# Optimization experiments

Measured on AMD Instinct MI355X. Metric: run time of the kernel, lower is better.

The kernel has to match this reference:

```python
import jax, jax.numpy as jnp
import numpy as np

NUM_HEADS = 8
HEAD_DIM = 64
SCALE = HEAD_DIM ** -0.5
EPS = 1e-5
STRIDE = (2, 2)


def _layernorm(x, g, b):
    mu = x.mean(-1, keepdims=True)
    var = x.var(-1, keepdims=True)
    return (x - mu) * jax.lax.rsqrt(var + EPS) * g + b


def _pool(t, convw, ln_g, ln_b, H):
    # t: (B, T, nh, 1 + H*H, d); depthwise-conv pool of spatial tokens, cls kept as-is,
    # LayerNorm over per-head channel dim applied after re-attaching cls (matches torch).
    B, T, nh, N, d = t.shape
    t = t.reshape(B * T, nh, N, d)
    cls_tok, body = t[:, :, :1], t[:, :, 1:]
    xs = body.reshape(B * T * nh, H, H, d)
    xs = jax.lax.conv_general_dilated(
        xs, convw, window_strides=STRIDE, padding=((1, 1), (1, 1)),
        dimension_numbers=('NHWC', 'HWIO', 'NHWC'), feature_group_count=d)
    Ho, Wo = xs.shape[1], xs.shape[2]
    xs = xs.reshape(B * T, nh, Ho * Wo, d)
    xs = jnp.concatenate([cls_tok, xs], axis=2)
    xs = _layernorm(xs, ln_g, ln_b)
    return xs.reshape(B, T, nh, Ho * Wo + 1, d), (Ho, Wo)


def _lin(t, w, b):
    # (B, T, nh, n, d) -> fold heads -> Linear(nh*d -> nh*d) -> unfold heads
    B, T, nh, n, d = t.shape
    y = t.transpose(0, 1, 3, 2, 4).reshape(B * T, n, nh * d)
    y = y @ w.T + b
    return y.reshape(B, T, n, nh, d).transpose(0, 1, 3, 2, 4)


def reference(x, x_ref, w_q, b_q, w_k, b_k, w_v, b_v, w_proj, b_proj,
              convw_q, convw_k, convw_v, ln_g_q, ln_b_q, ln_g_k, ln_b_k,
              ln_g_v, ln_b_v, rel_pos_h, rel_pos_w, hw_shape):
    B, T1, N, C = x.shape
    T2 = x_ref.shape[1]
    nh, d = NUM_HEADS, C // NUM_HEADS
    H = int(hw_shape)
    # pool_first: split heads before pooling;  q from x, k = v from x_ref
    q = x.reshape(B, T1, N, nh, d).transpose(0, 1, 3, 2, 4)
    kv = x_ref.reshape(B, T2, N, nh, d).transpose(0, 1, 3, 2, 4)
    q, q_shape = _pool(q, convw_q, ln_g_q, ln_b_q, H)
    k, k_shape = _pool(kv, convw_k, ln_g_k, ln_b_k, H)
    v, _ = _pool(kv, convw_v, ln_g_v, ln_b_v, H)
    q = _lin(q, w_q, b_q)
    k = _lin(k, w_k, b_k)
    v = _lin(v, w_v, b_v)
    # b t nh n d -> b nh (t n) d
    q = q.transpose(0, 2, 1, 3, 4).reshape(B, nh, -1, d)
    k = k.transpose(0, 2, 1, 3, 4).reshape(B, nh, -1, d)
    v = v.transpose(0, 2, 1, 3, 4).reshape(B, nh, -1, d)
    attn = jnp.einsum('bhqd,bhkd->bhqk', q * SCALE, k)
    # inline spatial relative position bias (uses UNSCALED q, as in torch source)
    qh, qw = q_shape
    kh, kw = k_shape
    dh = (np.arange(qh)[:, None] * max(kh / qh, 1.0)
          - np.arange(kh)[None, :] * max(qh / kh, 1.0)
          + (kh - 1) * max(qh / kh, 1.0)).astype(np.int32)
    dw = (np.arange(qw)[:, None] * max(kw / qw, 1.0)
          - np.arange(kw)[None, :] * max(qw / kw, 1.0)
          + (kw - 1) * max(qw / kw, 1.0)).astype(np.int32)
    Rh = rel_pos_h[dh]  # (qh, kh, d)
    Rw = rel_pos_w[dw]  # (qw, kw, d)
    r_q = q[:, :, 1:].reshape(B, nh, qh, qw, d)
    rel_h = jnp.einsum('byhwc,hkc->byhwk', r_q, Rh)
    rel_w = jnp.einsum('byhwc,wkc->byhwk', r_q, Rw)
    bias = (rel_h[..., :, None] + rel_w[..., None, :]).reshape(B, nh, qh * qw, kh * kw)
    attn = attn.at[:, :, 1:, 1:].add(bias)
    attn = jax.nn.softmax(attn, axis=-1)
    out = jnp.einsum('bhqk,bhkd->bhqd', attn, v)
    # residual pooling (skips cls token)
    out = out.at[:, :, 1:, :].add(q[:, :, 1:, :])
    qN = out.shape[2]
    out = out.transpose(0, 2, 1, 3).reshape(B, qN, nh * d)
    out = out @ w_proj.T + b_proj
    return out.reshape(B, T1, qN // T1, nh * d)


def setup_inputs() -> dict:
    key = jax.random.key(0)
    ks = jax.random.split(key, 16)
    B, T, H, C = 8, 1, 56, 512
    nh, d = NUM_HEADS, HEAD_DIM
    N = H * H + 1
    rel_dim = 2 * (H // 2) - 1  # 55
    f32 = jnp.float32
    return {
        'x': jax.random.normal(ks[0], (B, T, N, C), f32),
        'x_ref': jax.random.normal(ks[1], (B, T, N, C), f32),
        'w_q': jax.random.normal(ks[2], (C, C), f32) * 0.02,
        'b_q': jnp.zeros((C,), f32),
        'w_k': jax.random.normal(ks[3], (C, C), f32) * 0.02,
        'b_k': jnp.zeros((C,), f32),
        'w_v': jax.random.normal(ks[4], (C, C), f32) * 0.02,
        'b_v': jnp.zeros((C,), f32),
        'w_proj': jax.random.normal(ks[5], (C, C), f32) * 0.02,
        'b_proj': jnp.zeros((C,), f32),
        'convw_q': jax.random.normal(ks[6], (3, 3, 1, d), f32) * 0.1,
        'convw_k': jax.random.normal(ks[7], (3, 3, 1, d), f32) * 0.1,
        'convw_v': jax.random.normal(ks[8], (3, 3, 1, d), f32) * 0.1,
        'ln_g_q': jnp.ones((d,), f32), 'ln_b_q': jnp.zeros((d,), f32),
        'ln_g_k': jnp.ones((d,), f32), 'ln_b_k': jnp.zeros((d,), f32),
        'ln_g_v': jnp.ones((d,), f32), 'ln_b_v': jnp.zeros((d,), f32),
        'rel_pos_h': jax.random.normal(ks[9], (rel_dim, d), f32) * 0.02,
        'rel_pos_w': jax.random.normal(ks[10], (rel_dim, d), f32) * 0.02,
        'hw_shape': 56,
    }
```

## Files before the change

### kernel.cpp

```cpp
#include <hip/hip_runtime.h>

#define NH    8
#define DH    64
#define NTOK  3137
#define NOUT  785
#define CDIM  512
#define ROWS  6280
#define HO    28
#define HIN   56
#define NKT   13
#define RELD  55

typedef unsigned short u16;
typedef __attribute__((ext_vector_type(8))) short bf16x8;
typedef __attribute__((ext_vector_type(4))) float f32x4;

__device__ __forceinline__ float b2f(u16 u) { return __uint_as_float(((unsigned)u) << 16); }
__device__ __forceinline__ u16 f2b(float f) {
  unsigned u = __float_as_uint(f);
  return (u16)((u + 0x7FFFu + ((u >> 16) & 1u)) >> 16);
}

__global__ __launch_bounds__(256) void pool_ln_kernel(
    const float* __restrict__ x, const float* __restrict__ xr,
    const float* __restrict__ cwq, const float* __restrict__ cwk, const float* __restrict__ cwv,
    const float* __restrict__ gq, const float* __restrict__ bq,
    const float* __restrict__ gk, const float* __restrict__ bk,
    const float* __restrict__ gv, const float* __restrict__ bv,
    u16* __restrict__ Pq, u16* __restrict__ Pk, u16* __restrict__ Pv)
{
  int n     = blockIdx.x * 4 + (threadIdx.x >> 6);
  int bh    = blockIdx.y;
  int which = blockIdx.z;
  if (n >= NOUT) return;
  int b = bh >> 3, h = bh & 7;
  int di = threadIdx.x & 63;

  const float* src = (which == 0) ? x : xr;
  size_t srcbase = (size_t)b * NTOK * CDIM + (size_t)h * DH + di;
  size_t obase = (size_t)(b * NOUT + n) * CDIM + h * DH + di;

  float vq = 0.f, vk = 0.f;
  const float* cw0 = (which == 0) ? cwq : cwk;

  if (n == 0) {
    float t = src[srcbase];
    vq = t; vk = t;
  } else {
    int oy = (n - 1) / HO, ox = (n - 1) % HO;
#pragma unroll
    for (int ky = 0; ky < 3; ++ky) {
      int iy = oy * 2 - 1 + ky;
      if (iy < 0 || iy >= HIN) continue;
#pragma unroll
      for (int kx = 0; kx < 3; ++kx) {
        int ix = ox * 2 - 1 + kx;
        if (ix < 0 || ix >= HIN) continue;
        int tok = 1 + iy * HIN + ix;
        float t = src[srcbase + (size_t)tok * CDIM];
        vq += t * cw0[(ky * 3 + kx) * DH + di];
        if (which == 1) vk += t * cwv[(ky * 3 + kx) * DH + di];
      }
    }
  }

  {
    float s = vq, sq = vq * vq;
#pragma unroll
    for (int off = 32; off > 0; off >>= 1) {
      s  += __shfl_xor(s, off, 64);
      sq += __shfl_xor(sq, off, 64);
    }
    float mu  = s * (1.f / 64.f);
    float var = sq * (1.f / 64.f) - mu * mu;
    const float* g  = (which == 0) ? gq : gk;
    const float* be = (which == 0) ? bq : bk;
    float o = (vq - mu) * rsqrtf(var + 1e-5f) * g[di] + be[di];
    ((which == 0) ? Pq : Pk)[obase] = f2b(o);
  }
  if (which == 1) {
    float s = vk, sq = vk * vk;
#pragma unroll
    for (int off = 32; off > 0; off >>= 1) {
      s  += __shfl_xor(s, off, 64);
      sq += __shfl_xor(sq, off, 64);
    }
    float mu  = s * (1.f / 64.f);
    float var = sq * (1.f / 64.f) - mu * mu;
    float o = (vk - mu) * rsqrtf(var + 1e-5f) * gv[di] + bv[di];
    Pv[obase] = f2b(o);
  }
}

__global__ __launch_bounds__(256) void wcvt_kernel(
    const float* __restrict__ W0, const float* __restrict__ W1,
    const float* __restrict__ W2, const float* __restrict__ W3,
    u16* __restrict__ out)
{
  int idx = blockIdx.x * blockDim.x + threadIdx.x;
  const int per = CDIM * CDIM / 4;
  int mat = idx / per, off = (idx - mat * per) * 4;
  const float* src = (mat == 0) ? W0 : (mat == 1) ? W1 : (mat == 2) ? W2 : W3;
  float4 v = *(const float4*)(src + off);
  ushort4 o;
  o.x = f2b(v.x); o.y = f2b(v.y); o.z = f2b(v.z); o.w = f2b(v.w);
  *(ushort4*)(out + (size_t)mat * (CDIM * CDIM) + off) = o;
}

__global__ __launch_bounds__(256) void rcvt_kernel(
    const float* __restrict__ rph, const float* __restrict__ rpw,
    u16* __restrict__ Rhb, u16* __restrict__ Rwb)
{
  int idx = blockIdx.x * blockDim.x + threadIdx.x;
  if (idx >= 64 * 64) return;
  int r = idx >> 6, d = idx & 63;
  Rhb[idx] = (r < RELD) ? f2b(rph[r * DH + d]) : 0;
  Rwb[idx] = (r < RELD) ? f2b(rpw[r * DH + d]) : 0;
}

__global__ __launch_bounds__(256) void mgemm3_kernel(
    const u16* __restrict__ Xq, const u16* __restrict__ Xk, const u16* __restrict__ Xv,
    const u16* __restrict__ Wb, const float* __restrict__ bq,
    const float* __restrict__ bk, const float* __restrict__ bv,
    u16* __restrict__ Yq, u16* __restrict__ Yk, u16* __restrict__ Yv)
{
  int z = blockIdx.z;
  const u16* X = (z == 0) ? Xq : (z == 1) ? Xk : Xv;
  const u16* W = Wb + (size_t)z * CDIM * CDIM;
  const float* bias = (z == 0) ? bq : (z == 1) ? bk : bv;
  u16* Y = (z == 0) ? Yq : (z == 1) ? Yk : Yv;

  int tid = threadIdx.x;
  int w = tid >> 6, lane = tid & 63, l15 = lane & 15, lg = lane >> 4;
  int m0 = blockIdx.x * 128 + (w >> 1) * 64;
  int n0 = blockIdx.y * 128 + (w & 1) * 64;

  f32x4 acc[4][4] = {};
  float bs[4];
#pragma unroll
  for (int nf = 0; nf < 4; ++nf) bs[nf] = bias[n0 + nf * 16 + l15];

  for (int k0 = 0; k0 < CDIM; k0 += 32) {
    bf16x8 a[4], b[4];
#pragma unroll
    for (int mf = 0; mf < 4; ++mf) {
      int r = m0 + mf * 16 + l15;
      if (r > ROWS - 1) r = ROWS - 1;
      a[mf] = *(const bf16x8*)(X + (size_t)r * CDIM + k0 + lg * 8);
    }
#pragma unroll
    for (int nf = 0; nf < 4; ++nf) {
      int co = n0 + nf * 16 + l15;
      b[nf] = *(const bf16x8*)(W + (size_t)co * CDIM + k0 + lg * 8);
    }
#pragma unroll
    for (int mf = 0; mf < 4; ++mf)
#pragma unroll
      for (int nf = 0; nf < 4; ++nf)
        acc[mf][nf] = __builtin_amdgcn_mfma_f32_16x16x32_bf16(a[mf], b[nf], acc[mf][nf], 0, 0, 0);
  }

#pragma unroll
  for (int mf = 0; mf < 4; ++mf) {
#pragma unroll
    for (int j = 0; j < 4; ++j) {
      int r = m0 + mf * 16 + lg * 4 + j;
      if (r >= ROWS) continue;
      int bb = r / NOUT, n = r % NOUT;
#pragma unroll
      for (int nf = 0; nf < 4; ++nf) {
        int co = n0 + nf * 16 + l15;
        float v = acc[mf][nf][j] + bs[nf];
        Y[(((size_t)bb * NH + (co >> 6)) * NOUT + n) * DH + (co & 63)] = f2b(v);
      }
    }
  }
}

__global__ __launch_bounds__(256) void mgemm_proj_kernel(
    const u16* __restrict__ X, const u16* __restrict__ Wb, const float* __restrict__ bias,
    float* __restrict__ Y)
{
  int tid = threadIdx.x;
  int w = tid >> 6, lane = tid & 63, l15 = lane & 15, lg = lane >> 4;
  int m0 = blockIdx.x * 128 + (w >> 1) * 64;
  int n0 = blockIdx.y * 128 + (w & 1) * 64;

  f32x4 acc[4][4] = {};
  float bs[4];
#pragma unroll
  for (int nf = 0; nf < 4; ++nf) bs[nf] = bias[n0 + nf * 16 + l15];

  for (int k0 = 0; k0 < CDIM; k0 += 32) {
    bf16x8 a[4], b[4];
#pragma unroll
    for (int mf = 0; mf < 4; ++mf) {
      int r = m0 + mf * 16 + l15;
      if (r > ROWS - 1) r = ROWS - 1;
      a[mf] = *(const bf16x8*)(X + (size_t)r * CDIM + k0 + lg * 8);
    }
#pragma unroll
    for (int nf = 0; nf < 4; ++nf) {
      int co = n0 + nf * 16 + l15;
      b[nf] = *(const bf16x8*)(Wb + (size_t)co * CDIM + k0 + lg * 8);
    }
#pragma unroll
    for (int mf = 0; mf < 4; ++mf)
#pragma unroll
      for (int nf = 0; nf < 4; ++nf)
        acc[mf][nf] = __builtin_amdgcn_mfma_f32_16x16x32_bf16(a[mf], b[nf], acc[mf][nf], 0, 0, 0);
  }

#pragma unroll
  for (int mf = 0; mf < 4; ++mf) {
#pragma unroll
    for (int j = 0; j < 4; ++j) {
      int r = m0 + mf * 16 + lg * 4 + j;
      if (r >= ROWS) continue;
#pragma unroll
      for (int nf = 0; nf < 4; ++nf) {
        int co = n0 + nf * 16 + l15;
        Y[(size_t)r * CDIM + co] = acc[mf][nf][j] + bs[nf];
      }
    }
  }
}

__global__ __launch_bounds__(256, 4) void fattn_kernel(
    const u16* __restrict__ Q, const u16* __restrict__ K, const u16* __restrict__ V,
    const u16* __restrict__ Rhb, const u16* __restrict__ Rwb,
    u16* __restrict__ O)
{
  __shared__ u16 Vs[2][64][64];
  __shared__ u16 Ps[4][16][72];
  __shared__ u16 relh[64][57];
  __shared__ u16 relw[64][57];

  int bid = blockIdx.x;
  int nbid = (bid & 7) * 104 + (bid >> 3);
  int bh = nbid / NKT, qt = nbid % NKT;

  int tid = threadIdx.x;
  int w = tid >> 6, lane = tid & 63, l15 = lane & 15, lg = lane >> 4;
  size_t base = (size_t)bh * NOUT * DH;
  int q0 = qt * 64;

  int vkey_l = tid & 63;
  int vd0 = (tid >> 6) * 16;

  int qrow_qi = min(q0 + w * 16 + l15, NOUT - 1);
  const u16* qp = Q + base + (size_t)qrow_qi * DH + lg * 8;
  bf16x8 qa0 = *(const bf16x8*)(qp);
  bf16x8 qa1 = *(const bf16x8*)(qp + 32);

  {
    int key = min(vkey_l, NOUT - 1);
    const u16* vp = V + base + (size_t)key * DH + vd0;
    bf16x8 v0 = *(const bf16x8*)(vp);
    bf16x8 v1 = *(const bf16x8*)(vp + 8);
#pragma unroll
    for (int i = 0; i < 8; ++i) {
      int d = vd0 + i;
      Vs[0][d][((((vkey_l >> 3) ^ (d & 7)) << 3) | (vkey_l & 7))] = (u16)v0[i];
    }
#pragma unroll
    for (int i = 0; i < 8; ++i) {
      int d = vd0 + 8 + i;
      Vs[0][d][((((vkey_l >> 3) ^ (d & 7)) << 3) | (vkey_l & 7))] = (u16)v1[i];
    }
  }

#pragma unroll
  for (int nf = 0; nf < 4; ++nf) {
    int rr = nf * 16 + l15;
    const u16* hp = Rhb + rr * 64 + lg * 8;
    bf16x8 hb0 = *(const bf16x8*)(hp);
    bf16x8 hb1 = *(const bf16x8*)(hp + 32);
    f32x4 ah = {};
    ah = __builtin_amdgcn_mfma_f32_16x16x32_bf16(qa0, hb0, ah, 0, 0, 0);
    ah = __builtin_amdgcn_mfma_f32_16x16x32_bf16(qa1, hb1, ah, 0, 0, 0);
    const u16* wp = Rwb + rr * 64 + lg * 8;
    bf16x8 wb0 = *(const bf16x8*)(wp);
    bf16x8 wb1 = *(const bf16x8*)(wp + 32);
    f32x4 aw = {};
    aw = __builtin_amdgcn_mfma_f32_16x16x32_bf16(qa0, wb0, aw, 0, 0, 0);
    aw = __builtin_amdgcn_mfma_f32_16x16x32_bf16(qa1, wb1, aw, 0, 0, 0);
    if (rr < 57) {
#pragma unroll
      for (int j = 0; j < 4; ++j) {
        relh[w * 16 + lg * 4 + j][rr] = f2b(ah[j]);
        relw[w * 16 + lg * 4 + j][rr] = f2b(aw[j]);
      }
    }
  }

  int qy_j[4], qx_j[4];
  bool qv_j[4];
#pragma unroll
  for (int j = 0; j < 4; ++j) {
    int qi = q0 + w * 16 + lg * 4 + j;
    qv_j[j] = (qi >= 1);
    int qm1 = qi - 1;
    qy_j[j] = qm1 / HO;
    qx_j[j] = qm1 % HO;
  }

  f32x4 o0 = {}, o1 = {}, o2 = {}, o3 = {};
  float mrow[4], lrow[4];
#pragma unroll
  for (int j = 0; j < 4; ++j) { mrow[j] = -1e30f; lrow[j] = 0.f; }

  for (int t = 0; t < NKT; ++t) {
    int k0 = t * 64;
    int cur = t & 1;
    __syncthreads();

    bf16x8 nv0, nv1;
    bool have_next = (t + 1 < NKT);
    if (have_next) {
      int key = min(k0 + 64 + vkey_l, NOUT - 1);
      const u16* vp = V + base + (size_t)key * DH + vd0;
      nv0 = *(const bf16x8*)(vp);
      nv1 = *(const bf16x8*)(vp + 8);
    }

    bf16x8 kb[4][2];
#pragma unroll
    for (int sub = 0; sub < 4; ++sub) {
      int key = k0 + sub * 16 + l15;
      int keff = min(key, NOUT - 1);
      const u16* kp = K + base + (size_t)keff * DH + lg * 8;
      kb[sub][0] = *(const bf16x8*)(kp);
      kb[sub][1] = *(const bf16x8*)(kp + 32);
    }

    f32x4 s[4];
#pragma unroll
    for (int sub = 0; sub < 4; ++sub) {
      int key = k0 + sub * 16 + l15;
      f32x4 acc = {};
      acc = __builtin_amdgcn_mfma_f32_16x16x32_bf16(qa0, kb[sub][0], acc, 0, 0, 0);
      acc = __builtin_amdgcn_mfma_f32_16x16x32_bf16(qa1, kb[sub][1], acc, 0, 0, 0);
      bool kv = key < NOUT;
      int km1 = key - 1;
      int ky = km1 / HO, kx = km1 % HO;
#pragma unroll
      for (int j = 0; j < 4; ++j) {
        float v = acc[j] * 0.125f;
        if (key >= 1 && kv && qv_j[j]) {
          int ql = w * 16 + lg * 4 + j;
          v += b2f(relh[ql][qy_j[j] - ky + 27]) + b2f(relw[ql][qx_j[j] - kx + 27]);
        }
        if (!kv) v = -1e30f;
        s[sub][j] = v;
      }
    }

    if (have_next) {
#pragma unroll
      for (int i = 0; i < 8; ++i) {
        int d = vd0 + i;
        Vs[cur ^ 1][d][((((vkey_l >> 3) ^ (d & 7)) << 3) | (vkey_l & 7))] = (u16)nv0[i];
      }
#pragma unroll
      for (int i = 0; i < 8; ++i) {
        int d = vd0 + 8 + i;
        Vs[cur ^ 1][d][((((vkey_l >> 3) ^ (d & 7)) << 3) | (vkey_l & 7))] = (u16)nv1[i];
      }
    }

    float alpha[4];
#pragma unroll
    for (int j = 0; j < 4; ++j) {
      float lm = fmaxf(fmaxf(s[0][j], s[1][j]), fmaxf(s[2][j], s[3][j]));
      lm = fmaxf(lm, __shfl_xor(lm, 1));
      lm = fmaxf(lm, __shfl_xor(lm, 2));
      lm = fmaxf(lm, __shfl_xor(lm, 4));
      lm = fmaxf(lm, __shfl_xor(lm, 8));
      float mnew = fmaxf(mrow[j], lm);
      alpha[j] = __expf(mrow[j] - mnew);
      mrow[j] = mnew;
      float ps = 0.f;
#pragma unroll
      for (int sub = 0; sub < 4; ++sub) {
        float pv = __expf(s[sub][j] - mnew);
        s[sub][j] = pv;
        ps += pv;
      }
      ps += __shfl_xor(ps, 1);
      ps += __shfl_xor(ps, 2);
      ps += __shfl_xor(ps, 4);
      ps += __shfl_xor(ps, 8);
      lrow[j] = lrow[j] * alpha[j] + ps;
    }

#pragma unroll
    for (int j = 0; j < 4; ++j) {
      o0[j] *= alpha[j]; o1[j] *= alpha[j]; o2[j] *= alpha[j]; o3[j] *= alpha[j];
      Ps[w][lg * 4 + j][ 0 + l15] = f2b(s[0][j]);
      Ps[w][lg * 4 + j][16 + l15] = f2b(s[1][j]);
      Ps[w][lg * 4 + j][32 + l15] = f2b(s[2][j]);
      Ps[w][lg * 4 + j][48 + l15] = f2b(s[3][j]);
    }

    bf16x8 pa0 = *(const bf16x8*)&Ps[w][l15][lg * 8];
    bf16x8 pa1 = *(const bf16x8*)&Ps[w][l15][32 + lg * 8];
    {
      int r = 0 + l15;
      bf16x8 vb0 = *(const bf16x8*)&Vs[cur][r][((lg ^ (r & 7)) << 3)];
      bf16x8 vb1 = *(const bf16x8*)&Vs[cur][r][(((4 + lg) ^ (r & 7)) << 3)];
      o0 = __builtin_amdgcn_mfma_f32_16x16x32_bf16(pa0, vb0, o0, 0, 0, 0);
      o0 = __builtin_amdgcn_mfma_f32_16x16x32_bf16(pa1, vb1, o0, 0, 0, 0);
    }
    {
      int r = 16 + l15;
      bf16x8 vb0 = *(const bf16x8*)&Vs[cur][r][((lg ^ (r & 7)) << 3)];
      bf16x8 vb1 = *(const bf16x8*)&Vs[cur][r][(((4 + lg) ^ (r & 7)) << 3)];
      o1 = __builtin_amdgcn_mfma_f32_16x16x32_bf16(pa0, vb0, o1, 0, 0, 0);
      o1 = __builtin_amdgcn_mfma_f32_16x16x32_bf16(pa1, vb1, o1, 0, 0, 0);
    }
    {
      int r = 32 + l15;
      bf16x8 vb0 = *(const bf16x8*)&Vs[cur][r][((lg ^ (r & 7)) << 3)];
      bf16x8 vb1 = *(const bf16x8*)&Vs[cur][r][(((4 + lg) ^ (r & 7)) << 3)];
      o2 = __builtin_amdgcn_mfma_f32_16x16x32_bf16(pa0, vb0, o2, 0, 0, 0);
      o2 = __builtin_amdgcn_mfma_f32_16x16x32_bf16(pa1, vb1, o2, 0, 0, 0);
    }
    {
      int r = 48 + l15;
      bf16x8 vb0 = *(const bf16x8*)&Vs[cur][r][((lg ^ (r & 7)) << 3)];
      bf16x8 vb1 = *(const bf16x8*)&Vs[cur][r][(((4 + lg) ^ (r & 7)) << 3)];
      o3 = __builtin_amdgcn_mfma_f32_16x16x32_bf16(pa0, vb0, o3, 0, 0, 0);
      o3 = __builtin_amdgcn_mfma_f32_16x16x32_bf16(pa1, vb1, o3, 0, 0, 0);
    }
  }

  int b = bh >> 3, h = bh & 7;
#pragma unroll
  for (int j = 0; j < 4; ++j) {
    int ql = w * 16 + lg * 4 + j;
    int qi = q0 + ql;
    if (qi >= NOUT) continue;
    float inv = 1.f / lrow[j];
    float v0 = o0[j] * inv, v1 = o1[j] * inv, v2 = o2[j] * inv, v3 = o3[j] * inv;
    if (qi > 0) {
      const u16* qp2 = Q + base + (size_t)qi * DH;
      v0 += b2f(qp2[ 0 + l15]);
      v1 += b2f(qp2[16 + l15]);
      v2 += b2f(qp2[32 + l15]);
      v3 += b2f(qp2[48 + l15]);
    }
    size_t ob = ((size_t)b * NOUT + qi) * CDIM + h * DH;
    O[ob +  0 + l15] = f2b(v0);
    O[ob + 16 + l15] = f2b(v1);
    O[ob + 32 + l15] = f2b(v2);
    O[ob + 48 + l15] = f2b(v3);
  }
}

extern "C" void kernel_launch(void* const* d_in, const int* in_sizes, int n_in,
                              void* d_out, int out_size, void* d_ws, size_t ws_size,
                              hipStream_t stream) {
  const float* x     = (const float*)d_in[0];
  const float* xr    = (const float*)d_in[1];
  const float* wq    = (const float*)d_in[2];
  const float* bq    = (const float*)d_in[3];
  const float* wk    = (const float*)d_in[4];
  const float* bk    = (const float*)d_in[5];
  const float* wv    = (const float*)d_in[6];
  const float* bv    = (const float*)d_in[7];
  const float* wpj   = (const float*)d_in[8];
  const float* bpj   = (const float*)d_in[9];
  const float* cwq   = (const float*)d_in[10];
  const float* cwk   = (const float*)d_in[11];
  const float* cwv   = (const float*)d_in[12];
  const float* gq    = (const float*)d_in[13];
  const float* lbq   = (const float*)d_in[14];
  const float* gk    = (const float*)d_in[15];
  const float* lbk   = (const float*)d_in[16];
  const float* gv    = (const float*)d_in[17];
  const float* lbv   = (const float*)d_in[18];
  const float* rph   = (const float*)d_in[19];
  const float* rpw   = (const float*)d_in[20];
  (void)in_sizes; (void)n_in; (void)out_size; (void)ws_size;

  u16* ws = (u16*)d_ws;
  const size_t PSZ = (size_t)ROWS * CDIM;
  const size_t WSZ = (size_t)CDIM * CDIM;
  u16* ws0 = ws + 0 * PSZ;
  u16* ws1 = ws + 1 * PSZ;
  u16* ws2 = ws + 2 * PSZ;
  u16* ws3 = ws + 3 * PSZ;
  u16* ws4 = ws + 4 * PSZ;
  u16* Wb  = ws + 5 * PSZ;
  u16* Rhb = ws + 5 * PSZ + 4 * WSZ;
  u16* Rwb = Rhb + 64 * 64;
  u16* qbuf = (u16*)d_out;

  pool_ln_kernel<<<dim3((NOUT + 3) / 4, 64, 2), 256, 0, stream>>>(
      x, xr, cwq, cwk, cwv, gq, lbq, gk, lbk, gv, lbv, ws0, ws1, ws2);

  wcvt_kernel<<<(4 * CDIM * CDIM / 4 + 255) / 256, 256, 0, stream>>>(wq, wk, wv, wpj, Wb);
  rcvt_kernel<<<16, 256, 0, stream>>>(rph, rpw, Rhb, Rwb);

  dim3 g3((ROWS + 127) / 128, CDIM / 128, 3);
  mgemm3_kernel<<<g3, 256, 0, stream>>>(ws0, ws1, ws2, Wb, bq, bk, bv, qbuf, ws3, ws4);

  fattn_kernel<<<NKT * 64, 256, 0, stream>>>(qbuf, ws3, ws4, Rhb, Rwb, ws0);

  dim3 ggrid((ROWS + 127) / 128, CDIM / 128);
  mgemm_proj_kernel<<<ggrid, 256, 0, stream>>>(ws0, Wb + 3 * WSZ, bpj, (float*)d_out);
}
```

Measured before the change: 243.4 us.

## Split attention key range into two halves with a separate combine kernel

Each query tile's attention is now split across two blocks that cover key tiles 0-6 and 7-12. Each block writes unnormalized partial outputs plus its running max and sum, and a new fcomb kernel merges the two halves, normalizes, and adds the residual. Alongside this, the V double buffer becomes a single buffer with an extra barrier per tile so more blocks fit per CU, and the key row/column indices are updated incrementally instead of divided each tile. This doubles the grid to improve occupancy, at the cost of an extra launch, partial-result traffic, bf16 rounding of the partials, and an uneven split (7 vs 6 tiles).

```diff
diff --git a/kernel.cpp b/kernel.cpp
--- a/kernel.cpp
+++ b/kernel.cpp
@@ -226,19 +226,22 @@
   }
 }
 
-__global__ __launch_bounds__(256, 4) void fattn_kernel(
+__global__ __launch_bounds__(256, 5) void fattn_kernel(
     const u16* __restrict__ Q, const u16* __restrict__ K, const u16* __restrict__ V,
     const u16* __restrict__ Rhb, const u16* __restrict__ Rwb,
-    u16* __restrict__ O)
-{
-  __shared__ u16 Vs[2][64][64];
+    u16* __restrict__ PO, float* __restrict__ PML)
+{
+  __shared__ u16 Vs[64][64];
   __shared__ u16 Ps[4][16][72];
-  __shared__ u16 relh[64][57];
-  __shared__ u16 relw[64][57];
+  __shared__ u16 relh[64][RELD];
+  __shared__ u16 relw[64][RELD];
 
   int bid = blockIdx.x;
-  int nbid = (bid & 7) * 104 + (bid >> 3);
-  int bh = nbid / NKT, qt = nbid % NKT;
+  int nbid = (bid & 7) * 208 + (bid >> 3);
+  int bh = nbid / 26;
+  int r26 = nbid % 26;
+  int qt = r26 >> 1, half = r26 & 1;
+  int t0 = half ? 7 : 0, t1 = half ? NKT : 7;
 
   int tid = threadIdx.x;
   int w = tid >> 6, lane = tid & 63, l15 = lane & 15, lg = lane >> 4;
@@ -253,21 +256,12 @@
   bf16x8 qa0 = *(const bf16x8*)(qp);
   bf16x8 qa1 = *(const bf16x8*)(qp + 32);
 
+  bf16x8 nv0, nv1;
   {
-    int key = min(vkey_l, NOUT - 1);
+    int key = min(t0 * 64 + vkey_l, NOUT - 1);
     const u16* vp = V + base + (size_t)key * DH + vd0;
-    bf16x8 v0 = *(const bf16x8*)(vp);
-    bf16x8 v1 = *(const bf16x8*)(vp + 8);
-#pragma unroll
-    for (int i = 0; i < 8; ++i) {
-      int d = vd0 + i;
-      Vs[0][d][((((vkey_l >> 3) ^ (d & 7)) << 3) | (vkey_l & 7))] = (u16)v0[i];
-    }
-#pragma unroll
-    for (int i = 0; i < 8; ++i) {
-      int d = vd0 + 8 + i;
-      Vs[0][d][((((vkey_l >> 3) ^ (d & 7)) << 3) | (vkey_l & 7))] = (u16)v1[i];
-    }
+    nv0 = *(const bf16x8*)(vp);
+    nv1 = *(const bf16x8*)(vp + 8);
   }
 
 #pragma unroll
@@ -285,7 +279,7 @@
     f32x4 aw = {};
     aw = __builtin_amdgcn_mfma_f32_16x16x32_bf16(qa0, wb0, aw, 0, 0, 0);
     aw = __builtin_amdgcn_mfma_f32_16x16x32_bf16(qa1, wb1, aw, 0, 0, 0);
-    if (rr < 57) {
+    if (rr < RELD) {
 #pragma unroll
       for (int j = 0; j < 4; ++j) {
         relh[w * 16 + lg * 4 + j][rr] = f2b(ah[j]);
@@ -305,19 +299,36 @@
     qx_j[j] = qm1 % HO;
   }
 
+  int kyr[4], kxr[4];
+#pragma unroll
+  for (int sub = 0; sub < 4; ++sub) {
+    int km1 = t0 * 64 + sub * 16 + l15 - 1;
+    kyr[sub] = km1 / HO;
+    kxr[sub] = km1 % HO;
+  }
+
   f32x4 o0 = {}, o1 = {}, o2 = {}, o3 = {};
   float mrow[4], lrow[4];
 #pragma unroll
   for (int j = 0; j < 4; ++j) { mrow[j] = -1e30f; lrow[j] = 0.f; }
 
-  for (int t = 0; t < NKT; ++t) {
+  for (int t = t0; t < t1; ++t) {
     int k0 = t * 64;
-    int cur = t & 1;
     __syncthreads();
 
-    bf16x8 nv0, nv1;
-    bool have_next = (t + 1 < NKT);
-    if (have_next) {
+#pragma unroll
+    for (int i = 0; i < 8; ++i) {
+      int d = vd0 + i;
+      Vs[d][((((vkey_l >> 3) ^ (d & 7)) << 3) | (vkey_l & 7))] = (u16)nv0[i];
+    }
+#pragma unroll
+    for (int i = 0; i < 8; ++i) {
+      int d = vd0 + 8 + i;
+      Vs[d][((((vkey_l >> 3) ^ (d & 7)) << 3) | (vkey_l & 7))] = (u16)nv1[i];
+    }
+    __syncthreads();
+
+    if (t + 1 < t1) {
       int key = min(k0 + 64 + vkey_l, NOUT - 1);
       const u16* vp = V + base + (size_t)key * DH + vd0;
       nv0 = *(const bf16x8*)(vp);
@@ -342,8 +353,7 @@
       acc = __builtin_amdgcn_mfma_f32_16x16x32_bf16(qa0, kb[sub][0], acc, 0, 0, 0);
       acc = __builtin_amdgcn_mfma_f32_16x16x32_bf16(qa1, kb[sub][1], acc, 0, 0, 0);
       bool kv = key < NOUT;
-      int km1 = key - 1;
-      int ky = km1 / HO, kx = km1 % HO;
+      int ky = kyr[sub], kx = kxr[sub];
 #pragma unroll
       for (int j = 0; j < 4; ++j) {
         float v = acc[j] * 0.125f;
@@ -356,17 +366,10 @@
       }
     }
 
-    if (have_next) {
-#pragma unroll
-      for (int i = 0; i < 8; ++i) {
-        int d = vd0 + i;
-        Vs[cur ^ 1][d][((((vkey_l >> 3) ^ (d & 7)) << 3) | (vkey_l & 7))] = (u16)nv0[i];
-      }
-#pragma unroll
-      for (int i = 0; i < 8; ++i) {
-        int d = vd0 + 8 + i;
-        Vs[cur ^ 1][d][((((vkey_l >> 3) ^ (d & 7)) << 3) | (vkey_l & 7))] = (u16)nv1[i];
-      }
+#pragma unroll
+    for (int sub = 0; sub < 4; ++sub) {
+      kxr[sub] += 8; kyr[sub] += 2;
+      if (kxr[sub] >= HO) { kxr[sub] -= HO; kyr[sub] += 1; }
     }
 
     float alpha[4];
@@ -407,54 +410,78 @@
     bf16x8 pa1 = *(const bf16x8*)&Ps[w][l15][32 + lg * 8];
     {
       int r = 0 + l15;
-      bf16x8 vb0 = *(const bf16x8*)&Vs[cur][r][((lg ^ (r & 7)) << 3)];
-      bf16x8 vb1 = *(const bf16x8*)&Vs[cur][r][(((4 + lg) ^ (r & 7)) << 3)];
+      bf16x8 vb0 = *(const bf16x8*)&Vs[r][((lg ^ (r & 7)) << 3)];
+      bf16x8 vb1 = *(const bf16x8*)&Vs[r][(((4 + lg) ^ (r & 7)) << 3)];
       o0 = __builtin_amdgcn_mfma_f32_16x16x32_bf16(pa0, vb0, o0, 0, 0, 0);
       o0 = __builtin_amdgcn_mfma_f32_16x16x32_bf16(pa1, vb1, o0, 0, 0, 0);
     }
     {
       int r = 16 + l15;
-      bf16x8 vb0 = *(const bf16x8*)&Vs[cur][r][((lg ^ (r & 7)) << 3)];
-      bf16x8 vb1 = *(const bf16x8*)&Vs[cur][r][(((4 + lg) ^ (r & 7)) << 3)];
+      bf16x8 vb0 = *(const bf16x8*)&Vs[r][((lg ^ (r & 7)) << 3)];
+      bf16x8 vb1 = *(const bf16x8*)&Vs[r][(((4 + lg) ^ (r & 7)) << 3)];
       o1 = __builtin_amdgcn_mfma_f32_16x16x32_bf16(pa0, vb0, o1, 0, 0, 0);
       o1 = __builtin_amdgcn_mfma_f32_16x16x32_bf16(pa1, vb1, o1, 0, 0, 0);
     }
     {
       int r = 32 + l15;
-      bf16x8 vb0 = *(const bf16x8*)&Vs[cur][r][((lg ^ (r & 7)) << 3)];
-      bf16x8 vb1 = *(const bf16x8*)&Vs[cur][r][(((4 + lg) ^ (r & 7)) << 3)];
+      bf16x8 vb0 = *(const bf16x8*)&Vs[r][((lg ^ (r & 7)) << 3)];
+      bf16x8 vb1 = *(const bf16x8*)&Vs[r][(((4 + lg) ^ (r & 7)) << 3)];
       o2 = __builtin_amdgcn_mfma_f32_16x16x32_bf16(pa0, vb0, o2, 0, 0, 0);
       o2 = __builtin_amdgcn_mfma_f32_16x16x32_bf16(pa1, vb1, o2, 0, 0, 0);
     }
     {
       int r = 48 + l15;
-      bf16x8 vb0 = *(const bf16x8*)&Vs[cur][r][((lg ^ (r & 7)) << 3)];
-      bf16x8 vb1 = *(const bf16x8*)&Vs[cur][r][(((4 + lg) ^ (r & 7)) << 3)];
+      bf16x8 vb0 = *(const bf16x8*)&Vs[r][((lg ^ (r & 7)) << 3)];
+      bf16x8 vb1 = *(const bf16x8*)&Vs[r][(((4 + lg) ^ (r & 7)) << 3)];
       o3 = __builtin_amdgcn_mfma_f32_16x16x32_bf16(pa0, vb0, o3, 0, 0, 0);
       o3 = __builtin_amdgcn_mfma_f32_16x16x32_bf16(pa1, vb1, o3, 0, 0, 0);
     }
   }
 
-  int b = bh >> 3, h = bh & 7;
+  u16* oP = PO + (((size_t)(half * 64 + bh) * NKT + qt) << 12);
+  float* mlP = PML + (((size_t)(half * 64 + bh) * NKT + qt) << 7);
 #pragma unroll
   for (int j = 0; j < 4; ++j) {
     int ql = w * 16 + lg * 4 + j;
-    int qi = q0 + ql;
-    if (qi >= NOUT) continue;
-    float inv = 1.f / lrow[j];
-    float v0 = o0[j] * inv, v1 = o1[j] * inv, v2 = o2[j] * inv, v3 = o3[j] * inv;
-    if (qi > 0) {
-      const u16* qp2 = Q + base + (size_t)qi * DH;
-      v0 += b2f(qp2[ 0 + l15]);
-      v1 += b2f(qp2[16 + l15]);
-      v2 += b2f(qp2[32 + l15]);
-      v3 += b2f(qp2[48 + l15]);
-    }
-    size_t ob = ((size_t)b * NOUT + qi) * CDIM + h * DH;
-    O[ob +  0 + l15] = f2b(v0);
-    O[ob + 16 + l15] = f2b(v1);
-    O[ob + 32 + l15] = f2b(v2);
-    O[ob + 48 + l15] = f2b(v3);
+    if (l15 == 0) { mlP[ql] = mrow[j]; mlP[64 + ql] = lrow[j]; }
+    size_t ob = (size_t)ql * 64;
+    oP[ob +  0 + l15] = f2b(o0[j]);
+    oP[ob + 16 + l15] = f2b(o1[j]);
+    oP[ob + 32 + l15] = f2b(o2[j]);
+    oP[ob + 48 + l15] = f2b(o3[j]);
+  }
+}
+
+__global__ __launch_bounds__(256) void fcomb_kernel(
+    const u16* __restrict__ PO, const float* __restrict__ PML,
+    const u16* __restrict__ Q, u16* __restrict__ Oout)
+{
+  int qt = blockIdx.x, bh = blockIdx.y;
+  int tid = threadIdx.x;
+  int q = tid >> 2, d0 = (tid & 3) * 16;
+  int qi = qt * 64 + q;
+  if (qi >= NOUT) return;
+
+  size_t idx0 = (size_t)bh * NKT + qt;
+  size_t idx1 = (size_t)(64 + bh) * NKT + qt;
+  const float* ml0 = PML + (idx0 << 7);
+  const float* ml1 = PML + (idx1 << 7);
+  float m0 = ml0[q], l0 = ml0[64 + q];
+  float m1 = ml1[q], l1 = ml1[64 + q];
+  float m = fmaxf(m0, m1);
+  float a0 = __expf(m0 - m), a1 = __expf(m1 - m);
+  float inv = 1.f / (l0 * a0 + l1 * a1);
+
+  const u16* o0p = PO + (idx0 << 12) + (size_t)q * 64 + d0;
+  const u16* o1p = PO + (idx1 << 12) + (size_t)q * 64 + d0;
+  const u16* qp  = Q + (size_t)bh * NOUT * DH + (size_t)qi * DH + d0;
+  int b = bh >> 3, h = bh & 7;
+  u16* op = Oout + ((size_t)(b * NOUT) + qi) * CDIM + h * DH + d0;
+#pragma unroll
+  for (int i = 0; i < 16; ++i) {
+    float o = (b2f(o0p[i]) * a0 + b2f(o1p[i]) * a1) * inv;
+    if (qi > 0) o += b2f(qp[i]);
+    op[i] = f2b(o);
   }
 }
 
@@ -487,27 +514,33 @@
   u16* ws = (u16*)d_ws;
   const size_t PSZ = (size_t)ROWS * CDIM;
   const size_t WSZ = (size_t)CDIM * CDIM;
-  u16* ws0 = ws + 0 * PSZ;
-  u16* ws1 = ws + 1 * PSZ;
-  u16* ws2 = ws + 2 * PSZ;
-  u16* ws3 = ws + 3 * PSZ;
-  u16* ws4 = ws + 4 * PSZ;
-  u16* Wb  = ws + 5 * PSZ;
-  u16* Rhb = ws + 5 * PSZ + 4 * WSZ;
+  const size_t OSZ = (size_t)64 * NKT * 64 * 64;
+  const size_t MLSZ = (size_t)64 * NKT * 128;
+  u16* s0 = ws + 0 * PSZ;
+  u16* s1 = ws + 1 * PSZ;
+  u16* s2 = ws + 2 * PSZ;
+  u16* s3 = ws + 3 * PSZ;
+  u16* PO = ws + 4 * PSZ;
+  float* PML = (float*)(ws + 4 * PSZ + 2 * OSZ);
+  u16* Wb  = ws + 4 * PSZ + 2 * OSZ + 4 * MLSZ;
+  u16* Rhb = Wb + 4 * WSZ;
   u16* Rwb = Rhb + 64 * 64;
-  u16* qbuf = (u16*)d_out;
+  u16* qb1 = (u16*)d_out;
+  u16* qb2 = qb1 + PSZ;
 
   pool_ln_kernel<<<dim3((NOUT + 3) / 4, 64, 2), 256, 0, stream>>>(
-      x, xr, cwq, cwk, cwv, gq, lbq, gk, lbk, gv, lbv, ws0, ws1, ws2);
+      x, xr, cwq, cwk, cwv, gq, lbq, gk, lbk, gv, lbv, qb2, s0, s1);
 
   wcvt_kernel<<<(4 * CDIM * CDIM / 4 + 255) / 256, 256, 0, stream>>>(wq, wk, wv, wpj, Wb);
   rcvt_kernel<<<16, 256, 0, stream>>>(rph, rpw, Rhb, Rwb);
 
   dim3 g3((ROWS + 127) / 128, CDIM / 128, 3);
-  mgemm3_kernel<<<g3, 256, 0, stream>>>(ws0, ws1, ws2, Wb, bq, bk, bv, qbuf, ws3, ws4);
-
-  fattn_kernel<<<NKT * 64, 256, 0, stream>>>(qbuf, ws3, ws4, Rhb, Rwb, ws0);
+  mgemm3_kernel<<<g3, 256, 0, stream>>>(qb2, s0, s1, Wb, bq, bk, bv, qb1, s2, s3);
+
+  fattn_kernel<<<NKT * 64 * 2, 256, 0, stream>>>(qb1, s2, s3, Rhb, Rwb, PO, PML);
+
+  fcomb_kernel<<<dim3(NKT, 64), 256, 0, stream>>>(PO, PML, qb1, s0);
 
   dim3 ggrid((ROWS + 127) / 128, CDIM / 128);
-  mgemm_proj_kernel<<<ggrid, 256, 0, stream>>>(ws0, Wb + 3 * WSZ, bpj, (float*)d_out);
-}
+  mgemm_proj_kernel<<<ggrid, 256, 0, stream>>>(s0, Wb + 3 * WSZ, bpj, (float*)d_out);
+}
```

After: 322.8 us. 32.6% more time.

## Halve GEMM row tiles and hoist key-position div/mod out of attention loop

Applied to the files above, without the earlier changes.

Both MFMA GEMM kernels now use 64-row tiles instead of 128, which doubles the grid to spread the small GEMMs over more CUs, at the cost of more redundant weight loads. The attention kernel precomputes each key's y/x grid coordinates once and advances them incrementally per tile, replacing an integer divide and modulo per sub-tile. The rel-pos LDS tables shrink to 55 columns, which changes the row stride and therefore the bank pattern. The workspace pointers are also renamed.

```diff
diff --git a/kernel.cpp b/kernel.cpp
--- a/kernel.cpp
+++ b/kernel.cpp
@@ -132,18 +132,18 @@
 
   int tid = threadIdx.x;
   int w = tid >> 6, lane = tid & 63, l15 = lane & 15, lg = lane >> 4;
-  int m0 = blockIdx.x * 128 + (w >> 1) * 64;
+  int m0 = blockIdx.x * 64 + (w >> 1) * 32;
   int n0 = blockIdx.y * 128 + (w & 1) * 64;
 
-  f32x4 acc[4][4] = {};
+  f32x4 acc[2][4] = {};
   float bs[4];
 #pragma unroll
   for (int nf = 0; nf < 4; ++nf) bs[nf] = bias[n0 + nf * 16 + l15];
 
   for (int k0 = 0; k0 < CDIM; k0 += 32) {
-    bf16x8 a[4], b[4];
-#pragma unroll
-    for (int mf = 0; mf < 4; ++mf) {
+    bf16x8 a[2], b[4];
+#pragma unroll
+    for (int mf = 0; mf < 2; ++mf) {
       int r = m0 + mf * 16 + l15;
       if (r > ROWS - 1) r = ROWS - 1;
       a[mf] = *(const bf16x8*)(X + (size_t)r * CDIM + k0 + lg * 8);
@@ -154,14 +154,14 @@
       b[nf] = *(const bf16x8*)(W + (size_t)co * CDIM + k0 + lg * 8);
     }
 #pragma unroll
-    for (int mf = 0; mf < 4; ++mf)
+    for (int mf = 0; mf < 2; ++mf)
 #pragma unroll
       for (int nf = 0; nf < 4; ++nf)
         acc[mf][nf] = __builtin_amdgcn_mfma_f32_16x16x32_bf16(a[mf], b[nf], acc[mf][nf], 0, 0, 0);
   }
 
 #pragma unroll
-  for (int mf = 0; mf < 4; ++mf) {
+  for (int mf = 0; mf < 2; ++mf) {
 #pragma unroll
     for (int j = 0; j < 4; ++j) {
       int r = m0 + mf * 16 + lg * 4 + j;
@@ -183,18 +183,18 @@
 {
   int tid = threadIdx.x;
   int w = tid >> 6, lane = tid & 63, l15 = lane & 15, lg = lane >> 4;
-  int m0 = blockIdx.x * 128 + (w >> 1) * 64;
+  int m0 = blockIdx.x * 64 + (w >> 1) * 32;
   int n0 = blockIdx.y * 128 + (w & 1) * 64;
 
-  f32x4 acc[4][4] = {};
+  f32x4 acc[2][4] = {};
   float bs[4];
 #pragma unroll
   for (int nf = 0; nf < 4; ++nf) bs[nf] = bias[n0 + nf * 16 + l15];
 
   for (int k0 = 0; k0 < CDIM; k0 += 32) {
-    bf16x8 a[4], b[4];
-#pragma unroll
-    for (int mf = 0; mf < 4; ++mf) {
+    bf16x8 a[2], b[4];
+#pragma unroll
+    for (int mf = 0; mf < 2; ++mf) {
       int r = m0 + mf * 16 + l15;
       if (r > ROWS - 1) r = ROWS - 1;
       a[mf] = *(const bf16x8*)(X + (size_t)r * CDIM + k0 + lg * 8);
@@ -205,14 +205,14 @@
       b[nf] = *(const bf16x8*)(Wb + (size_t)co * CDIM + k0 + lg * 8);
     }
 #pragma unroll
-    for (int mf = 0; mf < 4; ++mf)
+    for (int mf = 0; mf < 2; ++mf)
 #pragma unroll
       for (int nf = 0; nf < 4; ++nf)
         acc[mf][nf] = __builtin_amdgcn_mfma_f32_16x16x32_bf16(a[mf], b[nf], acc[mf][nf], 0, 0, 0);
   }
 
 #pragma unroll
-  for (int mf = 0; mf < 4; ++mf) {
+  for (int mf = 0; mf < 2; ++mf) {
 #pragma unroll
     for (int j = 0; j < 4; ++j) {
       int r = m0 + mf * 16 + lg * 4 + j;
@@ -233,8 +233,8 @@
 {
   __shared__ u16 Vs[2][64][64];
   __shared__ u16 Ps[4][16][72];
-  __shared__ u16 relh[64][57];
-  __shared__ u16 relw[64][57];
+  __shared__ u16 relh[64][RELD];
+  __shared__ u16 relw[64][RELD];
 
   int bid = blockIdx.x;
   int nbid = (bid & 7) * 104 + (bid >> 3);
@@ -285,7 +285,7 @@
     f32x4 aw = {};
     aw = __builtin_amdgcn_mfma_f32_16x16x32_bf16(qa0, wb0, aw, 0, 0, 0);
     aw = __builtin_amdgcn_mfma_f32_16x16x32_bf16(qa1, wb1, aw, 0, 0, 0);
-    if (rr < 57) {
+    if (rr < RELD) {
 #pragma unroll
       for (int j = 0; j < 4; ++j) {
         relh[w * 16 + lg * 4 + j][rr] = f2b(ah[j]);
@@ -303,6 +303,14 @@
     int qm1 = qi - 1;
     qy_j[j] = qm1 / HO;
     qx_j[j] = qm1 % HO;
+  }
+
+  int kyr[4], kxr[4];
+#pragma unroll
+  for (int sub = 0; sub < 4; ++sub) {
+    int km1 = sub * 16 + l15 - 1;
+    kyr[sub] = km1 / HO;
+    kxr[sub] = km1 % HO;
   }
 
   f32x4 o0 = {}, o1 = {}, o2 = {}, o3 = {};
@@ -342,8 +350,7 @@
       acc = __builtin_amdgcn_mfma_f32_16x16x32_bf16(qa0, kb[sub][0], acc, 0, 0, 0);
       acc = __builtin_amdgcn_mfma_f32_16x16x32_bf16(qa1, kb[sub][1], acc, 0, 0, 0);
       bool kv = key < NOUT;
-      int km1 = key - 1;
-      int ky = km1 / HO, kx = km1 % HO;
+      int ky = kyr[sub], kx = kxr[sub];
 #pragma unroll
       for (int j = 0; j < 4; ++j) {
         float v = acc[j] * 0.125f;
@@ -354,6 +361,12 @@
         if (!kv) v = -1e30f;
         s[sub][j] = v;
       }
+    }
+
+#pragma unroll
+    for (int sub = 0; sub < 4; ++sub) {
+      kxr[sub] += 8; kyr[sub] += 2;
+      if (kxr[sub] >= HO) { kxr[sub] -= HO; kyr[sub] += 1; }
     }
 
     if (have_next) {
@@ -487,27 +500,27 @@
   u16* ws = (u16*)d_ws;
   const size_t PSZ = (size_t)ROWS * CDIM;
   const size_t WSZ = (size_t)CDIM * CDIM;
-  u16* ws0 = ws + 0 * PSZ;
-  u16* ws1 = ws + 1 * PSZ;
-  u16* ws2 = ws + 2 * PSZ;
-  u16* ws3 = ws + 3 * PSZ;
-  u16* ws4 = ws + 4 * PSZ;
+  u16* s0 = ws + 0 * PSZ;
+  u16* s1 = ws + 1 * PSZ;
+  u16* s2 = ws + 2 * PSZ;
+  u16* s3 = ws + 3 * PSZ;
+  u16* s4 = ws + 4 * PSZ;
   u16* Wb  = ws + 5 * PSZ;
-  u16* Rhb = ws + 5 * PSZ + 4 * WSZ;
+  u16* Rhb = Wb + 4 * WSZ;
   u16* Rwb = Rhb + 64 * 64;
   u16* qbuf = (u16*)d_out;
 
   pool_ln_kernel<<<dim3((NOUT + 3) / 4, 64, 2), 256, 0, stream>>>(
-      x, xr, cwq, cwk, cwv, gq, lbq, gk, lbk, gv, lbv, ws0, ws1, ws2);
+      x, xr, cwq, cwk, cwv, gq, lbq, gk, lbk, gv, lbv, s0, s1, s2);
 
   wcvt_kernel<<<(4 * CDIM * CDIM / 4 + 255) / 256, 256, 0, stream>>>(wq, wk, wv, wpj, Wb);
   rcvt_kernel<<<16, 256, 0, stream>>>(rph, rpw, Rhb, Rwb);
 
-  dim3 g3((ROWS + 127) / 128, CDIM / 128, 3);
-  mgemm3_kernel<<<g3, 256, 0, stream>>>(ws0, ws1, ws2, Wb, bq, bk, bv, qbuf, ws3, ws4);
-
-  fattn_kernel<<<NKT * 64, 256, 0, stream>>>(qbuf, ws3, ws4, Rhb, Rwb, ws0);
-
-  dim3 ggrid((ROWS + 127) / 128, CDIM / 128);
-  mgemm_proj_kernel<<<ggrid, 256, 0, stream>>>(ws0, Wb + 3 * WSZ, bpj, (float*)d_out);
-}
+  dim3 g3((ROWS + 63) / 64, CDIM / 128, 3);
+  mgemm3_kernel<<<g3, 256, 0, stream>>>(s0, s1, s2, Wb, bq, bk, bv, qbuf, s3, s4);
+
+  fattn_kernel<<<NKT * 64, 256, 0, stream>>>(qbuf, s3, s4, Rhb, Rwb, s0);
+
+  dim3 gp((ROWS + 63) / 64, CDIM / 128);
+  mgemm_proj_kernel<<<gp, 256, 0, stream>>>(s0, Wb + 3 * WSZ, bpj, (float*)d_out);
+}
```

Result: faster. 218.3 us (-10.3%).
